# Kernel optimization log

Measured on AMD Instinct MI355X. Metric: run time of the kernel, lower is better.

Reference implementation:

```python
import math
import jax, jax.numpy as jnp
import numpy as np

N_LAYERS = 3

def _layer_masks(d):
    # Deterministic reproduction of generate_mask_matrix: mask_ratio = 0 for
    # layer < 2 else 1 - log(1/layer + 1); int(ratio*d) random dims zeroed.
    masks = []
    for layer in range(N_LAYERS):
        ratio = 0.0 if layer < 2 else 1.0 - math.log(1.0 / layer + 1.0)
        num_masked = int(ratio * d)
        perm = np.random.RandomState(layer).permutation(d)
        masks.append(jnp.asarray((perm >= num_masked).astype(np.float32)))
    return masks


def setup_inputs() -> dict:
    key = jax.random.key(0)
    ks = jax.random.split(key, 12)
    U, I, R, D, E, B = 50000, 50000, 5, 64, 1000000, 8192
    N = U + I
    return {
        "users": jax.random.randint(ks[0], (B,), 0, U, dtype=jnp.int32),
        "items": jax.random.randint(ks[1], (B,), 0, I, dtype=jnp.int32),
        "user_emb": jax.random.normal(ks[2], (U, D), dtype=jnp.float32) * 0.01,
        "item_emb": jax.random.normal(ks[3], (I, D), dtype=jnp.float32) * 0.01,
        "rating_emb": jax.random.normal(ks[4], (R, D), dtype=jnp.float32) * 0.01,
        "W1": jax.random.normal(ks[5], (R, 2 * D, D), dtype=jnp.float32) * (1.0 / math.sqrt(2 * D)),
        "b1": jnp.zeros((R, D), dtype=jnp.float32),
        "W2": jax.random.normal(ks[6], (R, D, D), dtype=jnp.float32) * (1.0 / math.sqrt(D)),
        "b2": jnp.zeros((R, D), dtype=jnp.float32),
        "rows": jax.random.randint(ks[7], (R, E), 0, N, dtype=jnp.int32),
        "cols": jax.random.randint(ks[8], (R, E), 0, N, dtype=jnp.int32),
        # normalized-adjacency-like positive values (~1/avg_degree)
        "vals": jax.random.uniform(ks[9], (R, E), dtype=jnp.float32) * 0.1,
    }


def reference(users, items, user_emb, item_emb, rating_emb, W1, b1, W2, b2, rows, cols, vals):
    U = user_emb.shape[0]
    N = U + item_emb.shape[0]
    R, D = rating_emb.shape
    masks = _layer_masks(D)

    base = jnp.concatenate([user_emb, item_emb], axis=0)  # [N, D]
    group_outs = []
    for r in range(R):  # fixed small set of rating groups
        # per-rating attention MLP on cat([emb, rating_emb_r])
        t = jnp.concatenate([base, jnp.broadcast_to(rating_emb[r], (N, D))], axis=1)  # [N, 2D]
        h = jax.nn.leaky_relu(t @ W1[r] + b1[r]) @ W2[r] + b2[r]  # [N, D]
        acc = h
        prev = h
        for layer in range(N_LAYERS):
            # sparse A @ prev via gather + segment_sum
            agg = jax.ops.segment_sum(vals[r][:, None] * prev[cols[r]], rows[r], num_segments=N)
            m = masks[layer]
            prev = agg * m + prev * (1.0 - m)  # diag-mask residual combine
            acc = acc + prev
        group_outs.append(acc)

    out = jnp.mean(jnp.stack(group_outs, axis=1), axis=1)  # agg == 'mean'
    users_emb = out[users]
    items_emb = out[U + items]
    return (users_emb * items_emb).sum(1)  # is_mlp = False
```

## Files before the change

kernel.cpp:

```cpp
#include <hip/hip_runtime.h>
#include <hip/hip_bf16.h>
#include <cstdint>
#include <cstddef>

#define KEYSHIFT 20
#define COLMASK 0xFFFFFu
#define EPB 8192
#define SUB 4096
#define BSHIFT 8
#define NRB 256
#define CCAP 3072

typedef short bf16x8 __attribute__((ext_vector_type(8)));
typedef float f32x4 __attribute__((ext_vector_type(4)));

__device__ __forceinline__ unsigned short f2bf(float f) {
    uint32_t u = __float_as_uint(f);
    u += ((u >> 16) & 1u) + 0x7fffu;
    return (unsigned short)(u >> 16);
}
__device__ __forceinline__ float bf2f(unsigned short h) {
    return __uint_as_float(((uint32_t)h) << 16);
}

static uint64_t compute_mask_bits() {
    uint32_t mt[624];
    mt[0] = 2u;
    for (int i = 1; i < 624; i++)
        mt[i] = 1812433253u * (mt[i - 1] ^ (mt[i - 1] >> 30)) + (uint32_t)i;
    int mti = 624;
    auto genrand = [&]() -> uint32_t {
        if (mti >= 624) {
            for (int k = 0; k < 624; k++) {
                uint32_t y = (mt[k] & 0x80000000u) | (mt[(k + 1) % 624] & 0x7fffffffu);
                mt[k] = mt[(k + 397) % 624] ^ (y >> 1) ^ ((y & 1u) ? 2567483615u : 0u);
            }
            mti = 0;
        }
        uint32_t y = mt[mti++];
        y ^= y >> 11;
        y ^= (y << 7) & 2636928640u;
        y ^= (y << 15) & 4022730752u;
        y ^= y >> 18;
        return y;
    };
    int arr[64];
    for (int i = 0; i < 64; i++) arr[i] = i;
    for (int i = 63; i >= 1; i--) {
        uint32_t mask = (uint32_t)i;
        mask |= mask >> 1; mask |= mask >> 2; mask |= mask >> 4;
        mask |= mask >> 8; mask |= mask >> 16;
        uint32_t v;
        do { v = genrand() & mask; } while (v > (uint32_t)i);
        int tmp = arr[i]; arr[i] = arr[v]; arr[v] = tmp;
    }
    uint64_t bits = 0;
    for (int d = 0; d < 64; d++)
        if (arr[d] >= 38) bits |= (1ull << d);
    return bits;
}

__global__ void flag_kernel(const int* __restrict__ users, const int* __restrict__ items,
                            unsigned char* __restrict__ flag, int B, int U) {
    int i = blockIdx.x * 256 + threadIdx.x;
    if (i < B) flag[users[i]] = 1;
    else if (i < 2 * B) flag[U + items[i - B]] = 1;
}

__global__ void flist_kernel(const unsigned char* __restrict__ flag,
                             int* __restrict__ flist, int* __restrict__ fcount, int n) {
    int i = blockIdx.x * 256 + threadIdx.x;
    if (i < n && flag[i]) {
        int p = atomicAdd(fcount, 1);
        flist[p] = i;
    }
}

__global__ void c1_kernel(const float* __restrict__ rating_emb, const float* __restrict__ W1,
                          const float* __restrict__ b1, float* __restrict__ c1_all) {
    int r = blockIdx.x;
    int t = threadIdx.x;
    const float* W1r = W1 + (size_t)r * (128 * 64);
    float acc = b1[r * 64 + t];
    for (int k = 0; k < 64; k++)
        acc += rating_emb[r * 64 + k] * W1r[(64 + k) * 64 + t];
    c1_all[r * 64 + t] = acc;
}

__global__ void packw_kernel(const float* __restrict__ W1, const float* __restrict__ W2,
                             short* __restrict__ wpack) {
    int r = blockIdx.x;
    int t = threadIdx.x;
    const float* W1r = W1 + (size_t)r * (128 * 64);
    const float* W2r = W2 + (size_t)r * (64 * 64);
    for (int e = t; e < 2 * 4 * 2 * 64 * 8; e += 256) {
        int i = e & 7;
        int lane = (e >> 3) & 63;
        int kc = (e >> 9) & 1;
        int ct = (e >> 10) & 3;
        int g = (e >> 12) & 1;
        int k = kc * 32 + ((lane >> 4) << 3) + i;
        int col = (ct << 4) + (lane & 15);
        float w = (g == 0) ? W1r[k * 64 + col] : W2r[k * 64 + col];
        unsigned short hi = f2bf(w);
        unsigned short lo = f2bf(w - bf2f(hi));
        size_t fb = ((((size_t)r * 2 + g) * 4 + ct) * 2 + kc) * 2;
        wpack[(fb + 0) * 512 + lane * 8 + i] = (short)hi;
        wpack[(fb + 1) * 512 + lane * 8 + i] = (short)lo;
    }
}

__global__ __launch_bounds__(1024) void bucket_count_kernel(
    const int* __restrict__ rows, int* __restrict__ gcnt,
    int* __restrict__ blockBase, int E, int K, int nb) {
    __shared__ int hist[2048];
    int r = blockIdx.y, blk = blockIdx.x, t = threadIdx.x;
    for (int i = t; i < K; i += 1024) hist[i] = 0;
    __syncthreads();
    size_t base = (size_t)r * E + (size_t)blk * EPB;
    int cnt = E - blk * EPB;
    if (cnt > EPB) cnt = EPB;
    for (int k = t; k < cnt; k += 1024)
        atomicAdd(&hist[rows[base + k] >> BSHIFT], 1);
    __syncthreads();
    for (int i = t; i < K; i += 1024) {
        int c = hist[i];
        int bb = (c > 0) ? atomicAdd(&gcnt[r * K + i], c) : 0;
        blockBase[((size_t)r * nb + blk) * K + i] = bb;
    }
}

__global__ void bucket_scan_kernel(const int* __restrict__ gcnt,
                                   int* __restrict__ bptr, int K) {
    __shared__ int sh[256];
    int r = blockIdx.x;
    int t = threadIdx.x;
    int base = t * 8;
    int v[8];
    int s = 0;
    #pragma unroll
    for (int j = 0; j < 8; j++) {
        int idx = base + j;
        v[j] = (idx < K) ? gcnt[r * K + idx] : 0;
        s += v[j];
    }
    sh[t] = s;
    __syncthreads();
    for (int off = 1; off < 256; off <<= 1) {
        int x = (t >= off) ? sh[t - off] : 0;
        __syncthreads();
        sh[t] += x;
        __syncthreads();
    }
    int run = sh[t] - s;
    #pragma unroll
    for (int j = 0; j < 8; j++) {
        int idx = base + j;
        if (idx <= K) bptr[r * (K + 1) + idx] = run;
        run += v[j];
    }
}

__global__ __launch_bounds__(1024) void bucket_scatter_kernel(
    const int* __restrict__ rows, const int* __restrict__ cols,
    const float* __restrict__ vals, const int* __restrict__ bptr,
    const int* __restrict__ blockBase, uint2* __restrict__ rec,
    int E, int K, long long eStride, long long pStride,
    long long bbStride, long long rStride) {
    __shared__ uint2 staged[SUB];
    __shared__ int gaddr[SUB];
    __shared__ int cursor[512];
    __shared__ int lhist[512];
    __shared__ int aux[512];
    int r = blockIdx.y;
    const int* rows_r = rows + (size_t)r * eStride;
    const int* cols_r = cols + (size_t)r * eStride;
    const float* vals_r = vals + (size_t)r * eStride;
    const int* bptr_r = bptr + (size_t)r * pStride;
    const int* bb_r = blockBase + (size_t)r * bbStride;
    uint2* rec_r = rec + (size_t)r * rStride;
    int blk = blockIdx.x, t = threadIdx.x;
    if (t < 512)
        cursor[t] = (t < K) ? (bptr_r[t] + bb_r[(size_t)blk * K + t]) : 0;
    size_t base = (size_t)blk * EPB;
    int cnt = E - blk * EPB;
    if (cnt > EPB) cnt = EPB;
    for (int c0 = 0; c0 < cnt; c0 += SUB) {
        int scnt = cnt - c0;
        if (scnt > SUB) scnt = SUB;
        if (t < 512) lhist[t] = 0;
        __syncthreads();
        int bkt_[4], lpos_[4];
        uint2 rv_[4];
        #pragma unroll
        for (int q = 0; q < 4; q++) {
            int kk = (q << 10) + t;
            bkt_[q] = -1;
            if (kk < scnt) {
                size_t g = base + c0 + kk;
                int row = rows_r[g];
                int b = row >> BSHIFT;
                bkt_[q] = b;
                rv_[q] = make_uint2(((uint32_t)(row & (NRB - 1)) << KEYSHIFT) |
                                        (uint32_t)cols_r[g],
                                    __float_as_uint(vals_r[g]));
                lpos_[q] = atomicAdd(&lhist[b], 1);
            }
        }
        __syncthreads();
        int v = (t < 512) ? lhist[t] : 0;
        if (t < 512) aux[t] = v;
        __syncthreads();
        for (int off = 1; off < 512; off <<= 1) {
            int x = 0;
            if (t >= off && t < 512) x = aux[t - off];
            __syncthreads();
            if (t < 512) aux[t] += x;
            __syncthreads();
        }
        if (t < 512) {
            int ex = aux[t] - v;
            int gb = cursor[t];
            cursor[t] = gb + v;
            lhist[t] = ex;
            aux[t] = gb - ex;
        }
        __syncthreads();
        #pragma unroll
        for (int q = 0; q < 4; q++) {
            if (bkt_[q] >= 0) {
                int sidx = lhist[bkt_[q]] + lpos_[q];
                staged[sidx] = rv_[q];
                gaddr[sidx] = aux[bkt_[q]] + sidx;
            }
        }
        __syncthreads();
        for (int i = t; i < scnt; i += 1024)
            rec_r[gaddr[i]] = staged[i];
        __syncthreads();
    }
}

__global__ __launch_bounds__(1024) void bucket_scatter_legacy(
    const int* __restrict__ rows, const int* __restrict__ cols,
    const float* __restrict__ vals, const int* __restrict__ bptr,
    const int* __restrict__ blockBase, uint2* __restrict__ rec,
    int E, int K, long long eStride, long long pStride,
    long long bbStride, long long rStride) {
    __shared__ int cursor[2048];
    int r = blockIdx.y;
    const int* rows_r = rows + (size_t)r * eStride;
    const int* cols_r = cols + (size_t)r * eStride;
    const float* vals_r = vals + (size_t)r * eStride;
    const int* bptr_r = bptr + (size_t)r * pStride;
    const int* bb_r = blockBase + (size_t)r * bbStride;
    uint2* rec_r = rec + (size_t)r * rStride;
    int blk = blockIdx.x, t = threadIdx.x;
    for (int i = t; i < K; i += 1024)
        cursor[i] = bptr_r[i] + bb_r[(size_t)blk * K + i];
    __syncthreads();
    size_t base = (size_t)blk * EPB;
    int cnt = E - blk * EPB;
    if (cnt > EPB) cnt = EPB;
    for (int k = t; k < cnt; k += 1024) {
        int row = rows_r[base + k];
        int b = row >> BSHIFT;
        int pos = atomicAdd(&cursor[b], 1);
        uint32_t key = ((uint32_t)(row & (NRB - 1)) << KEYSHIFT) | (uint32_t)cols_r[base + k];
        rec_r[pos] = make_uint2(key, __float_as_uint(vals_r[base + k]));
    }
}

__global__ __launch_bounds__(256) void bucket_sort_kernel(
    const uint2* __restrict__ rec, uint2* __restrict__ srec,
    const int* __restrict__ bptr, int* __restrict__ rp, int K, int N,
    long long rStride, long long pStride, long long rpStride) {
    __shared__ uint2 staged[CCAP];
    __shared__ int hist[NRB];
    __shared__ int excl[NRB];
    int r = blockIdx.y;
    const uint2* rec_r = rec + (size_t)r * rStride;
    uint2* srec_r = srec + (size_t)r * rStride;
    const int* bptr_r = bptr + (size_t)r * pStride;
    int* rp_r = rp + (size_t)r * rpStride;
    int b = blockIdx.x;
    int t = threadIdx.x;
    hist[t] = 0;
    __syncthreads();
    int start = bptr_r[b], end = bptr_r[b + 1];
    int m = end - start;
    for (int e = start + t; e < end; e += 256)
        atomicAdd(&hist[rec_r[e].x >> KEYSHIFT], 1);
    __syncthreads();
    int v = hist[t];
    excl[t] = v;
    __syncthreads();
    for (int off = 1; off < 256; off <<= 1) {
        int x = (t >= off) ? excl[t - off] : 0;
        __syncthreads();
        excl[t] += x;
        __syncthreads();
    }
    int ex = excl[t] - v;
    excl[t] = ex;
    hist[t] = 0;
    int row = b * NRB + t;
    if (row < N) rp_r[row] = start + ex;
    if (b == K - 1 && t == 0) rp_r[N] = bptr_r[K];
    __syncthreads();
    if (m <= CCAP) {
        for (int e = start + t; e < end; e += 256) {
            uint2 rr = rec_r[e];
            int rel = (int)(rr.x >> KEYSHIFT);
            int pos = excl[rel] + atomicAdd(&hist[rel], 1);
            staged[pos] = rr;
        }
        __syncthreads();
        for (int i = t; i < m; i += 256)
            srec_r[start + i] = staged[i];
    } else {
        for (int e = start + t; e < end; e += 256) {
            uint2 rr = rec_r[e];
            int rel = (int)(rr.x >> KEYSHIFT);
            int pos = start + excl[rel] + atomicAdd(&hist[rel], 1);
            srec_r[pos] = rr;
        }
    }
}

__global__ __launch_bounds__(256) void mlp_kernel(
    const float* __restrict__ user_emb, const float* __restrict__ item_emb,
    const short* __restrict__ wpack, const float* __restrict__ c1_all,
    const float* __restrict__ b2,
    unsigned short* __restrict__ prev, long long prevStride,
    float* __restrict__ out_acc, const unsigned char* __restrict__ flag,
    int r0, int nr, int n_rows, int U, int init) {
    __shared__ float sT[64 * 68];

    int t = threadIdx.x;
    int wv = t >> 6;
    int l = t & 63;
    int row0 = blockIdx.x * 64;
    int arow = row0 + (wv << 4) + (l & 15);
    int kb = (l >> 4) << 3;
    int trow = (wv << 4) + (l & 15);

    bf16x8 xh0, xh1, xl0, xl1;
    {
        float xv[16];
        #pragma unroll
        for (int i = 0; i < 16; i++) xv[i] = 0.f;
        if (arow < n_rows) {
            const float* src = (arow < U) ? (user_emb + (size_t)arow * 64)
                                          : (item_emb + (size_t)(arow - U) * 64);
            float4 p0 = *(const float4*)(src + kb);
            float4 p1 = *(const float4*)(src + kb + 4);
            float4 p2 = *(const float4*)(src + 32 + kb);
            float4 p3 = *(const float4*)(src + 32 + kb + 4);
            xv[0] = p0.x; xv[1] = p0.y; xv[2] = p0.z; xv[3] = p0.w;
            xv[4] = p1.x; xv[5] = p1.y; xv[6] = p1.z; xv[7] = p1.w;
            xv[8] = p2.x; xv[9] = p2.y; xv[10] = p2.z; xv[11] = p2.w;
            xv[12] = p3.x; xv[13] = p3.y; xv[14] = p3.z; xv[15] = p3.w;
        }
        #pragma unroll
        for (int i = 0; i < 8; i++) {
            unsigned short hi = f2bf(xv[i]);
            xh0[i] = (short)hi;
            xl0[i] = (short)f2bf(xv[i] - bf2f(hi));
        }
        #pragma unroll
        for (int i = 0; i < 8; i++) {
            unsigned short hi = f2bf(xv[8 + i]);
            xh1[i] = (short)hi;
            xl1[i] = (short)f2bf(xv[8 + i] - bf2f(hi));
        }
    }

    int dr0 = row0 + (wv << 4) + ((l >> 4) << 2);
    bool va0 = (dr0 + 0) < n_rows, va1 = (dr0 + 1) < n_rows;
    bool va2 = (dr0 + 2) < n_rows, va3 = (dr0 + 3) < n_rows;
    bool fl0 = va0 && flag[dr0 + 0], fl1 = va1 && flag[dr0 + 1];
    bool fl2 = va2 && flag[dr0 + 2], fl3 = va3 && flag[dr0 + 3];
    float oa[16];
    #pragma unroll
    for (int i = 0; i < 16; i++) oa[i] = 0.f;

    for (int rr = r0; rr < r0 + nr; ++rr) {
        const short* wp1 = wpack + ((size_t)rr * 2 + 0) * 16 * 512;
        const short* wp2 = wpack + ((size_t)rr * 2 + 1) * 16 * 512;

        #pragma unroll
        for (int ct = 0; ct < 4; ct++) {
            float c1v = c1_all[rr * 64 + (ct << 4) + (l & 15)];
            f32x4 acc = {c1v, c1v, c1v, c1v};
            #pragma unroll
            for (int kc = 0; kc < 2; kc++) {
                const short* fb = wp1 + ((ct * 2 + kc) * 2) * 512 + l * 8;
                bf16x8 bh = *(const bf16x8*)(fb);
                bf16x8 bl = *(const bf16x8*)(fb + 512);
                bf16x8 ah = (kc == 0) ? xh0 : xh1;
                bf16x8 al = (kc == 0) ? xl0 : xl1;
                acc = __builtin_amdgcn_mfma_f32_16x16x32_bf16(ah, bh, acc, 0, 0, 0);
                acc = __builtin_amdgcn_mfma_f32_16x16x32_bf16(al, bh, acc, 0, 0, 0);
                acc = __builtin_amdgcn_mfma_f32_16x16x32_bf16(ah, bl, acc, 0, 0, 0);
            }
            #pragma unroll
            for (int i = 0; i < 4; i++) {
                float v = acc[i];
                v = (v >= 0.f) ? v : 0.01f * v;
                sT[((wv << 4) + ((l >> 4) << 2) + i) * 68 + (ct << 4) + (l & 15)] = v;
            }
        }
        bf16x8 th0, th1, tl0, tl1;
        {
            float4 t0 = *(const float4*)(sT + trow * 68 + kb);
            float4 t1 = *(const float4*)(sT + trow * 68 + kb + 4);
            float4 t2 = *(const float4*)(sT + trow * 68 + 32 + kb);
            float4 t3 = *(const float4*)(sT + trow * 68 + 32 + kb + 4);
            float tv[16] = {t0.x, t0.y, t0.z, t0.w, t1.x, t1.y, t1.z, t1.w,
                            t2.x, t2.y, t2.z, t2.w, t3.x, t3.y, t3.z, t3.w};
            #pragma unroll
            for (int i = 0; i < 8; i++) {
                unsigned short hi = f2bf(tv[i]);
                th0[i] = (short)hi;
                tl0[i] = (short)f2bf(tv[i] - bf2f(hi));
            }
            #pragma unroll
            for (int i = 0; i < 8; i++) {
                unsigned short hi = f2bf(tv[8 + i]);
                th1[i] = (short)hi;
                tl1[i] = (short)f2bf(tv[8 + i] - bf2f(hi));
            }
        }
        #pragma unroll
        for (int ct = 0; ct < 4; ct++) {
            float b2v = b2[rr * 64 + (ct << 4) + (l & 15)];
            f32x4 acc = {b2v, b2v, b2v, b2v};
            #pragma unroll
            for (int kc = 0; kc < 2; kc++) {
                const short* fb = wp2 + ((ct * 2 + kc) * 2) * 512 + l * 8;
                bf16x8 bh = *(const bf16x8*)(fb);
                bf16x8 bl = *(const bf16x8*)(fb + 512);
                bf16x8 ah = (kc == 0) ? th0 : th1;
                bf16x8 al = (kc == 0) ? tl0 : tl1;
                acc = __builtin_amdgcn_mfma_f32_16x16x32_bf16(ah, bh, acc, 0, 0, 0);
                acc = __builtin_amdgcn_mfma_f32_16x16x32_bf16(al, bh, acc, 0, 0, 0);
                acc = __builtin_amdgcn_mfma_f32_16x16x32_bf16(ah, bl, acc, 0, 0, 0);
            }
            unsigned short* pp = prev + (size_t)rr * prevStride + (ct << 4) + (l & 15);
            #pragma unroll
            for (int i = 0; i < 4; i++) {
                bool va = (i == 0) ? va0 : (i == 1) ? va1 : (i == 2) ? va2 : va3;
                bool fl = (i == 0) ? fl0 : (i == 1) ? fl1 : (i == 2) ? fl2 : fl3;
                if (va) {
                    float hv = acc[i];
                    pp[(size_t)(dr0 + i) * 64] = f2bf(hv);
                    if (fl) oa[ct * 4 + i] += hv;
                }
            }
        }
    }

    #pragma unroll
    for (int ct = 0; ct < 4; ct++) {
        #pragma unroll
        for (int i = 0; i < 4; i++) {
            bool fl = (i == 0) ? fl0 : (i == 1) ? fl1 : (i == 2) ? fl2 : fl3;
            if (fl) {
                float* o = out_acc + (size_t)(dr0 + i) * 64 + (ct << 4) + (l & 15);
                if (init) *o = oa[ct * 4 + i];
                else *o += oa[ct * 4 + i];
            }
        }
    }
}

__global__ __launch_bounds__(256) void spmm_kernel(
    const unsigned short* __restrict__ prev, unsigned short* __restrict__ next,
    float* __restrict__ out_acc, const int* __restrict__ rp,
    const uint2* __restrict__ rec, const unsigned char* __restrict__ flag, int n) {
    int wave = (int)((blockIdx.x * (unsigned)blockDim.x + threadIdx.x) >> 6);
    int lane = threadIdx.x & 63;
    int rA = wave * 2;
    if (rA >= n) return;
    int rB = rA + 1;
    int sub = lane >> 4;
    int dl = lane & 15;
    int sA = rp[rA], eA = rp[rA + 1];
    int sB = 0, eB = 0;
    if (rB < n) { sB = rp[rB]; eB = rp[rB + 1]; }
    float axA = 0.f, ayA = 0.f, azA = 0.f, awA = 0.f;
    float axB = 0.f, ayB = 0.f, azB = 0.f, awB = 0.f;
    int ewA = sA + sub, ewB = sB + sub;
    while (ewA < eA || ewB < eB) {
        int a1 = ewA + 4, a2 = ewA + 8, a3 = ewA + 12;
        int b1 = ewB + 4, b2 = ewB + 8, b3 = ewB + 12;
        uint2 ra0 = rec[ewA < eA ? ewA : 0];
        uint2 ra1 = rec[a1 < eA ? a1 : 0];
        uint2 ra2 = rec[a2 < eA ? a2 : 0];
        uint2 ra3 = rec[a3 < eA ? a3 : 0];
        uint2 rb0 = rec[ewB < eB ? ewB : 0];
        uint2 rb1 = rec[b1 < eB ? b1 : 0];
        uint2 rb2 = rec[b2 < eB ? b2 : 0];
        uint2 rb3 = rec[b3 < eB ? b3 : 0];
        float vA0 = (ewA < eA) ? __uint_as_float(ra0.y) : 0.f;
        float vA1 = (a1 < eA) ? __uint_as_float(ra1.y) : 0.f;
        float vA2 = (a2 < eA) ? __uint_as_float(ra2.y) : 0.f;
        float vA3 = (a3 < eA) ? __uint_as_float(ra3.y) : 0.f;
        float vB0 = (ewB < eB) ? __uint_as_float(rb0.y) : 0.f;
        float vB1 = (b1 < eB) ? __uint_as_float(rb1.y) : 0.f;
        float vB2 = (b2 < eB) ? __uint_as_float(rb2.y) : 0.f;
        float vB3 = (b3 < eB) ? __uint_as_float(rb3.y) : 0.f;
        ushort4 qa0 = *(const ushort4*)(prev + (size_t)(ra0.x & COLMASK) * 64 + dl * 4);
        ushort4 qa1 = *(const ushort4*)(prev + (size_t)(ra1.x & COLMASK) * 64 + dl * 4);
        ushort4 qa2 = *(const ushort4*)(prev + (size_t)(ra2.x & COLMASK) * 64 + dl * 4);
        ushort4 qa3 = *(const ushort4*)(prev + (size_t)(ra3.x & COLMASK) * 64 + dl * 4);
        ushort4 qb0 = *(const ushort4*)(prev + (size_t)(rb0.x & COLMASK) * 64 + dl * 4);
        ushort4 qb1 = *(const ushort4*)(prev + (size_t)(rb1.x & COLMASK) * 64 + dl * 4);
        ushort4 qb2 = *(const ushort4*)(prev + (size_t)(rb2.x & COLMASK) * 64 + dl * 4);
        ushort4 qb3 = *(const ushort4*)(prev + (size_t)(rb3.x & COLMASK) * 64 + dl * 4);
        axA += vA0 * bf2f(qa0.x) + vA1 * bf2f(qa1.x) + vA2 * bf2f(qa2.x) + vA3 * bf2f(qa3.x);
        ayA += vA0 * bf2f(qa0.y) + vA1 * bf2f(qa1.y) + vA2 * bf2f(qa2.y) + vA3 * bf2f(qa3.y);
        azA += vA0 * bf2f(qa0.z) + vA1 * bf2f(qa1.z) + vA2 * bf2f(qa2.z) + vA3 * bf2f(qa3.z);
        awA += vA0 * bf2f(qa0.w) + vA1 * bf2f(qa1.w) + vA2 * bf2f(qa2.w) + vA3 * bf2f(qa3.w);
        axB += vB0 * bf2f(qb0.x) + vB1 * bf2f(qb1.x) + vB2 * bf2f(qb2.x) + vB3 * bf2f(qb3.x);
        ayB += vB0 * bf2f(qb0.y) + vB1 * bf2f(qb1.y) + vB2 * bf2f(qb2.y) + vB3 * bf2f(qb3.y);
        azB += vB0 * bf2f(qb0.z) + vB1 * bf2f(qb1.z) + vB2 * bf2f(qb2.z) + vB3 * bf2f(qb3.z);
        awB += vB0 * bf2f(qb0.w) + vB1 * bf2f(qb1.w) + vB2 * bf2f(qb2.w) + vB3 * bf2f(qb3.w);
        ewA += 16; ewB += 16;
    }
    axA += __shfl_xor(axA, 16); ayA += __shfl_xor(ayA, 16);
    azA += __shfl_xor(azA, 16); awA += __shfl_xor(awA, 16);
    axA += __shfl_xor(axA, 32); ayA += __shfl_xor(ayA, 32);
    azA += __shfl_xor(azA, 32); awA += __shfl_xor(awA, 32);
    axB += __shfl_xor(axB, 16); ayB += __shfl_xor(ayB, 16);
    azB += __shfl_xor(azB, 16); awB += __shfl_xor(awB, 16);
    axB += __shfl_xor(axB, 32); ayB += __shfl_xor(ayB, 32);
    azB += __shfl_xor(azB, 32); awB += __shfl_xor(awB, 32);
    if (sub == 0) {
        ushort4 nv;
        nv.x = f2bf(axA); nv.y = f2bf(ayA); nv.z = f2bf(azA); nv.w = f2bf(awA);
        *(ushort4*)(next + (size_t)rA * 64 + dl * 4) = nv;
    } else if (sub == 1 && flag[rA]) {
        float* o = out_acc + (size_t)rA * 64 + dl * 4;
        float4 ov = *(const float4*)o;
        ov.x += axA; ov.y += ayA; ov.z += azA; ov.w += awA;
        *(float4*)o = ov;
    } else if (sub == 2 && rB < n) {
        ushort4 nv;
        nv.x = f2bf(axB); nv.y = f2bf(ayB); nv.z = f2bf(azB); nv.w = f2bf(awB);
        *(ushort4*)(next + (size_t)rB * 64 + dl * 4) = nv;
    } else if (sub == 3 && rB < n && flag[rB]) {
        float* o = out_acc + (size_t)rB * 64 + dl * 4;
        float4 ov = *(const float4*)o;
        ov.x += axB; ov.y += ayB; ov.z += azB; ov.w += awB;
        *(float4*)o = ov;
    }
}

__global__ __launch_bounds__(256) void spmm_masked_kernel(
    const unsigned short* __restrict__ prev, float* __restrict__ out_acc,
    const int* __restrict__ rp, const uint2* __restrict__ rec,
    unsigned long long maskbits, const int* __restrict__ flist,
    const int* __restrict__ fcount) {
    int wave = (int)((blockIdx.x * (unsigned)blockDim.x + threadIdx.x) >> 6);
    int lane = threadIdx.x & 63;
    int fc = *fcount;
    int w2 = wave * 2;
    if (w2 >= fc) return;
    int rowA = flist[w2];
    int rowB = (w2 + 1 < fc) ? flist[w2 + 1] : -1;
    int sub = lane >> 4;
    int dl = lane & 15;
    int sA = rp[rowA], eA = rp[rowA + 1];
    int sB = 0, eB = 0;
    if (rowB >= 0) { sB = rp[rowB]; eB = rp[rowB + 1]; }
    float axA = 0.f, ayA = 0.f, azA = 0.f, awA = 0.f;
    float axB = 0.f, ayB = 0.f, azB = 0.f, awB = 0.f;
    int ewA = sA + sub, ewB = sB + sub;
    while (ewA < eA || ewB < eB) {
        int a1 = ewA + 4, a2 = ewA + 8, a3 = ewA + 12;
        int b1 = ewB + 4, b2 = ewB + 8, b3 = ewB + 12;
        uint2 ra0 = rec[ewA < eA ? ewA : 0];
        uint2 ra1 = rec[a1 < eA ? a1 : 0];
        uint2 ra2 = rec[a2 < eA ? a2 : 0];
        uint2 ra3 = rec[a3 < eA ? a3 : 0];
        uint2 rb0 = rec[ewB < eB ? ewB : 0];
        uint2 rb1 = rec[b1 < eB ? b1 : 0];
        uint2 rb2 = rec[b2 < eB ? b2 : 0];
        uint2 rb3 = rec[b3 < eB ? b3 : 0];
        float vA0 = (ewA < eA) ? __uint_as_float(ra0.y) : 0.f;
        float vA1 = (a1 < eA) ? __uint_as_float(ra1.y) : 0.f;
        float vA2 = (a2 < eA) ? __uint_as_float(ra2.y) : 0.f;
        float vA3 = (a3 < eA) ? __uint_as_float(ra3.y) : 0.f;
        float vB0 = (ewB < eB) ? __uint_as_float(rb0.y) : 0.f;
        float vB1 = (b1 < eB) ? __uint_as_float(rb1.y) : 0.f;
        float vB2 = (b2 < eB) ? __uint_as_float(rb2.y) : 0.f;
        float vB3 = (b3 < eB) ? __uint_as_float(rb3.y) : 0.f;
        ushort4 qa0 = *(const ushort4*)(prev + (size_t)(ra0.x & COLMASK) * 64 + dl * 4);
        ushort4 qa1 = *(const ushort4*)(prev + (size_t)(ra1.x & COLMASK) * 64 + dl * 4);
        ushort4 qa2 = *(const ushort4*)(prev + (size_t)(ra2.x & COLMASK) * 64 + dl * 4);
        ushort4 qa3 = *(const ushort4*)(prev + (size_t)(ra3.x & COLMASK) * 64 + dl * 4);
        ushort4 qb0 = *(const ushort4*)(prev + (size_t)(rb0.x & COLMASK) * 64 + dl * 4);
        ushort4 qb1 = *(const ushort4*)(prev + (size_t)(rb1.x & COLMASK) * 64 + dl * 4);
        ushort4 qb2 = *(const ushort4*)(prev + (size_t)(rb2.x & COLMASK) * 64 + dl * 4);
        ushort4 qb3 = *(const ushort4*)(prev + (size_t)(rb3.x & COLMASK) * 64 + dl * 4);
        axA += vA0 * bf2f(qa0.x) + vA1 * bf2f(qa1.x) + vA2 * bf2f(qa2.x) + vA3 * bf2f(qa3.x);
        ayA += vA0 * bf2f(qa0.y) + vA1 * bf2f(qa1.y) + vA2 * bf2f(qa2.y) + vA3 * bf2f(qa3.y);
        azA += vA0 * bf2f(qa0.z) + vA1 * bf2f(qa1.z) + vA2 * bf2f(qa2.z) + vA3 * bf2f(qa3.z);
        awA += vA0 * bf2f(qa0.w) + vA1 * bf2f(qa1.w) + vA2 * bf2f(qa2.w) + vA3 * bf2f(qa3.w);
        axB += vB0 * bf2f(qb0.x) + vB1 * bf2f(qb1.x) + vB2 * bf2f(qb2.x) + vB3 * bf2f(qb3.x);
        ayB += vB0 * bf2f(qb0.y) + vB1 * bf2f(qb1.y) + vB2 * bf2f(qb2.y) + vB3 * bf2f(qb3.y);
        azB += vB0 * bf2f(qb0.z) + vB1 * bf2f(qb1.z) + vB2 * bf2f(qb2.z) + vB3 * bf2f(qb3.z);
        awB += vB0 * bf2f(qb0.w) + vB1 * bf2f(qb1.w) + vB2 * bf2f(qb2.w) + vB3 * bf2f(qb3.w);
        ewA += 16; ewB += 16;
    }
    axA += __shfl_xor(axA, 16); ayA += __shfl_xor(ayA, 16);
    azA += __shfl_xor(azA, 16); awA += __shfl_xor(awA, 16);
    axA += __shfl_xor(axA, 32); ayA += __shfl_xor(ayA, 32);
    azA += __shfl_xor(azA, 32); awA += __shfl_xor(awA, 32);
    axB += __shfl_xor(axB, 16); ayB += __shfl_xor(ayB, 16);
    azB += __shfl_xor(azB, 16); awB += __shfl_xor(awB, 16);
    axB += __shfl_xor(axB, 32); ayB += __shfl_xor(ayB, 32);
    azB += __shfl_xor(azB, 32); awB += __shfl_xor(awB, 32);
    if (sub == 0) {
        ushort4 pq = *(const ushort4*)(prev + (size_t)rowA * 64 + dl * 4);
        float px = bf2f(pq.x), py = bf2f(pq.y), pz = bf2f(pq.z), pw = bf2f(pq.w);
        float rx = ((maskbits >> (dl * 4 + 0)) & 1ull) ? axA : px;
        float ry = ((maskbits >> (dl * 4 + 1)) & 1ull) ? ayA : py;
        float rz = ((maskbits >> (dl * 4 + 2)) & 1ull) ? azA : pz;
        float rw = ((maskbits >> (dl * 4 + 3)) & 1ull) ? awA : pw;
        float* o = out_acc + (size_t)rowA * 64 + dl * 4;
        float4 ov = *(const float4*)o;
        ov.x += rx; ov.y += ry; ov.z += rz; ov.w += rw;
        *(float4*)o = ov;
    } else if (sub == 2 && rowB >= 0) {
        ushort4 pq = *(const ushort4*)(prev + (size_t)rowB * 64 + dl * 4);
        float px = bf2f(pq.x), py = bf2f(pq.y), pz = bf2f(pq.z), pw = bf2f(pq.w);
        float rx = ((maskbits >> (dl * 4 + 0)) & 1ull) ? axB : px;
        float ry = ((maskbits >> (dl * 4 + 1)) & 1ull) ? ayB : py;
        float rz = ((maskbits >> (dl * 4 + 2)) & 1ull) ? azB : pz;
        float rw = ((maskbits >> (dl * 4 + 3)) & 1ull) ? awB : pw;
        float* o = out_acc + (size_t)rowB * 64 + dl * 4;
        float4 ov = *(const float4*)o;
        ov.x += rx; ov.y += ry; ov.z += rz; ov.w += rw;
        *(float4*)o = ov;
    }
}

__global__ __launch_bounds__(256) void dot_kernel(
    const float* __restrict__ out_acc, const int* __restrict__ users,
    const int* __restrict__ items, float* __restrict__ out,
    int Bn, int U, float scale) {
    int w = (int)((blockIdx.x * (unsigned)blockDim.x + threadIdx.x) >> 6);
    int lane = threadIdx.x & 63;
    if (w >= Bn) return;
    int u = users[w], it = items[w];
    float a = out_acc[(size_t)u * 64 + lane];
    float c = out_acc[((size_t)(U + it)) * 64 + lane];
    float p = a * c;
    #pragma unroll
    for (int off = 32; off > 0; off >>= 1) p += __shfl_down(p, off);
    if (lane == 0) out[w] = p * scale;
}

extern "C" void kernel_launch(void* const* d_in, const int* in_sizes, int n_in,
                              void* d_out, int out_size, void* d_ws, size_t ws_size,
                              hipStream_t stream) {
    const int* users = (const int*)d_in[0];
    const int* items = (const int*)d_in[1];
    const float* user_emb = (const float*)d_in[2];
    const float* item_emb = (const float*)d_in[3];
    const float* rating_emb = (const float*)d_in[4];
    const float* W1 = (const float*)d_in[5];
    const float* b1 = (const float*)d_in[6];
    const float* W2 = (const float*)d_in[7];
    const float* b2 = (const float*)d_in[8];
    const int* rows = (const int*)d_in[9];
    const int* cols = (const int*)d_in[10];
    const float* vals = (const float*)d_in[11];
    float* out = (float*)d_out;

    const int Dd = 64;
    int U = in_sizes[2] / Dd;
    int I = in_sizes[3] / Dd;
    int R = in_sizes[4] / Dd;
    int N = U + I;
    int E = in_sizes[9] / R;
    int Bn = in_sizes[0];
    int K = (N + NRB - 1) / NRB;
    int nb = (E + EPB - 1) / EPB;

    auto al = [](size_t b) { return (b + 255) & ~(size_t)255; };
    size_t sliceA = al((size_t)N * 64 * 2);
    size_t bufA_all = al((size_t)R * N * 64 * 2);
    size_t wpack_sz = al((size_t)R * 2 * 4 * 2 * 2 * 64 * 8 * 2);
    size_t common = al((size_t)N * 64 * 4) + sliceA
        + al((size_t)R * K * 4)
        + al((size_t)R * (K + 1) * 4) + al((size_t)R * nb * K * 4)
        + al((size_t)R * (N + 1) * 4) + al((size_t)R * 64 * 4) + wpack_sz
        + al((size_t)N) + al((size_t)2 * Bn * 4) + al(4);
    size_t rec_one = al((size_t)E * 8);
    size_t rec_all = al((size_t)E * 8 * R);
    int mlpb = 0, batched = 0;
    if (ws_size >= common + bufA_all + 2 * rec_all + 65536) {
        mlpb = 1; batched = 1;
    } else if (ws_size >= common + sliceA + 2 * rec_all + 65536) {
        batched = 1;
    }
    size_t bufAsz = mlpb ? bufA_all : sliceA;
    size_t recsz = batched ? rec_all : rec_one;

    char* p = (char*)d_ws;
    auto carve = [&](size_t bytes) -> char* {
        char* q = p;
        p += (bytes + 255) & ~(size_t)255;
        return q;
    };
    float* out_acc = (float*)carve((size_t)N * 64 * 4);
    unsigned short* bufA = (unsigned short*)carve(bufAsz);
    unsigned short* bufB = (unsigned short*)carve(sliceA);
    uint2* rec = (uint2*)carve(recsz);
    uint2* srec = (uint2*)carve(recsz);
    int* gcnt = (int*)carve((size_t)R * K * 4);
    int* bptr = (int*)carve((size_t)R * (K + 1) * 4);
    int* blockBase = (int*)carve((size_t)R * nb * K * 4);
    int* row_ptr = (int*)carve((size_t)R * (N + 1) * 4);
    float* c1_all = (float*)carve((size_t)R * 64 * 4);
    short* wpack = (short*)carve(wpack_sz);
    unsigned char* flag = (unsigned char*)carve((size_t)N);
    int* flist = (int*)carve((size_t)2 * Bn * 4);
    int* fcount = (int*)carve(4);

    uint64_t maskbits = compute_mask_bits();

    hipMemsetAsync(flag, 0, (size_t)N, stream);
    hipMemsetAsync(fcount, 0, 4, stream);
    hipMemsetAsync(gcnt, 0, (size_t)R * K * 4, stream);

    flag_kernel<<<(2 * Bn + 255) / 256, 256, 0, stream>>>(users, items, flag, Bn, U);
    flist_kernel<<<(N + 255) / 256, 256, 0, stream>>>(flag, flist, fcount, N);
    c1_kernel<<<R, 64, 0, stream>>>(rating_emb, W1, b1, c1_all);
    packw_kernel<<<R, 256, 0, stream>>>(W1, W2, wpack);

    dim3 cgrid(nb, R);
    bucket_count_kernel<<<cgrid, 1024, 0, stream>>>(rows, gcnt, blockBase, E, K, nb);
    bucket_scan_kernel<<<R, 256, 0, stream>>>(gcnt, bptr, K);

    if (batched) {
        dim3 sgrid(nb, R);
        if (K <= 512)
            bucket_scatter_kernel<<<sgrid, 1024, 0, stream>>>(
                rows, cols, vals, bptr, blockBase, rec, E, K,
                (long long)E, (long long)(K + 1), (long long)nb * K, (long long)E);
        else
            bucket_scatter_legacy<<<sgrid, 1024, 0, stream>>>(
                rows, cols, vals, bptr, blockBase, rec, E, K,
                (long long)E, (long long)(K + 1), (long long)nb * K, (long long)E);
        dim3 ogrid(K, R);
        bucket_sort_kernel<<<ogrid, 256, 0, stream>>>(
            rec, srec, bptr, row_ptr, K, N,
            (long long)E, (long long)(K + 1), (long long)(N + 1));
    }

    if (mlpb)
        mlp_kernel<<<(N + 63) / 64, 256, 0, stream>>>(
            user_emb, item_emb, wpack, c1_all, b2,
            bufA, (long long)N * 64, out_acc, flag, 0, R, N, U, 1);

    int spmm_waves = (N + 1) / 2;
    int spmm_blocks = (spmm_waves + 3) / 4;
    int masked_blocks = (Bn + 3) / 4;
    for (int r = 0; r < R; r++) {
        const int* bptr_r = bptr + (size_t)r * (K + 1);
        int* rp_r = row_ptr + (size_t)r * (N + 1);
        uint2* srec_r = batched ? (srec + (size_t)r * E) : srec;
        unsigned short* prev_r = mlpb ? (bufA + (size_t)r * N * 64) : bufA;

        if (!batched) {
            dim3 sgrid(nb, 1);
            if (K <= 512)
                bucket_scatter_kernel<<<sgrid, 1024, 0, stream>>>(
                    rows + (size_t)r * E, cols + (size_t)r * E, vals + (size_t)r * E,
                    bptr_r, blockBase + (size_t)r * nb * K, rec, E, K, 0, 0, 0, 0);
            else
                bucket_scatter_legacy<<<sgrid, 1024, 0, stream>>>(
                    rows + (size_t)r * E, cols + (size_t)r * E, vals + (size_t)r * E,
                    bptr_r, blockBase + (size_t)r * nb * K, rec, E, K, 0, 0, 0, 0);
            dim3 ogrid(K, 1);
            bucket_sort_kernel<<<ogrid, 256, 0, stream>>>(
                rec, srec, bptr_r, rp_r, K, N, 0, 0, 0);
        }

        if (!mlpb)
            mlp_kernel<<<(N + 63) / 64, 256, 0, stream>>>(
                user_emb, item_emb, wpack, c1_all, b2,
                bufA, 0, out_acc, flag, r, 1, N, U, (r == 0) ? 1 : 0);

        spmm_kernel<<<spmm_blocks, 256, 0, stream>>>(prev_r, bufB, out_acc, rp_r,
                                                     srec_r, flag, N);
        spmm_kernel<<<spmm_blocks, 256, 0, stream>>>(bufB, prev_r, out_acc, rp_r,
                                                     srec_r, flag, N);
        spmm_masked_kernel<<<masked_blocks, 256, 0, stream>>>(prev_r, out_acc, rp_r,
                                                              srec_r, maskbits,
                                                              flist, fcount);
    }

    float scale = 1.0f / (float)(R * R);
    dot_kernel<<<(Bn * 64 + 255) / 256, 256, 0, stream>>>(out_acc, users, items, out,
                                                          Bn, U, scale);
}
```

Measured before the change: 667.4 us.

## Batch SpMM across all rating groups in a 2D grid with deferred accumulation

When the workspace is large enough, the SpMM and masked SpMM launches for all five rating groups are merged into single launches, with blockIdx.y selecting the group. The out_acc read-modify-write that each group used to do is dropped from those kernels. Per-group results stay in full bufA/bufB buffers plus a compact masked-output buffer, and a new final_sum kernel adds them into out_acc for the flagged rows. This removes per-group launch overhead and serialization and fills the GPU with more concurrent work. In exchange it needs much more workspace and adds one extra reduction kernel.

```diff
diff --git a/kernel.cpp b/kernel.cpp
--- a/kernel.cpp
+++ b/kernel.cpp
@@ -478,7 +478,13 @@
 __global__ __launch_bounds__(256) void spmm_kernel(
     const unsigned short* __restrict__ prev, unsigned short* __restrict__ next,
     float* __restrict__ out_acc, const int* __restrict__ rp,
-    const uint2* __restrict__ rec, const unsigned char* __restrict__ flag, int n) {
+    const uint2* __restrict__ rec, const unsigned char* __restrict__ flag, int n,
+    long long pvS, long long nxS, long long rpS, long long rcS, int doOut) {
+    int rr = blockIdx.y;
+    prev += (size_t)rr * pvS;
+    next += (size_t)rr * nxS;
+    rp += (size_t)rr * rpS;
+    rec += (size_t)rr * rcS;
     int wave = (int)((blockIdx.x * (unsigned)blockDim.x + threadIdx.x) >> 6);
     int lane = threadIdx.x & 63;
     int rA = wave * 2;
@@ -541,7 +547,7 @@
         ushort4 nv;
         nv.x = f2bf(axA); nv.y = f2bf(ayA); nv.z = f2bf(azA); nv.w = f2bf(awA);
         *(ushort4*)(next + (size_t)rA * 64 + dl * 4) = nv;
-    } else if (sub == 1 && flag[rA]) {
+    } else if (sub == 1 && doOut && flag[rA]) {
         float* o = out_acc + (size_t)rA * 64 + dl * 4;
         float4 ov = *(const float4*)o;
         ov.x += axA; ov.y += ayA; ov.z += azA; ov.w += awA;
@@ -550,7 +556,7 @@
         ushort4 nv;
         nv.x = f2bf(axB); nv.y = f2bf(ayB); nv.z = f2bf(azB); nv.w = f2bf(awB);
         *(ushort4*)(next + (size_t)rB * 64 + dl * 4) = nv;
-    } else if (sub == 3 && rB < n && flag[rB]) {
+    } else if (sub == 3 && doOut && rB < n && flag[rB]) {
         float* o = out_acc + (size_t)rB * 64 + dl * 4;
         float4 ov = *(const float4*)o;
         ov.x += axB; ov.y += ayB; ov.z += azB; ov.w += awB;
@@ -562,7 +568,14 @@
     const unsigned short* __restrict__ prev, float* __restrict__ out_acc,
     const int* __restrict__ rp, const uint2* __restrict__ rec,
     unsigned long long maskbits, const int* __restrict__ flist,
-    const int* __restrict__ fcount) {
+    const int* __restrict__ fcount,
+    unsigned short* __restrict__ mout, long long moS,
+    long long pvS, long long rpS, long long rcS, int doOut) {
+    int rr = blockIdx.y;
+    prev += (size_t)rr * pvS;
+    rp += (size_t)rr * rpS;
+    rec += (size_t)rr * rcS;
+    unsigned short* mo = mout + (size_t)rr * moS;
     int wave = (int)((blockIdx.x * (unsigned)blockDim.x + threadIdx.x) >> 6);
     int lane = threadIdx.x & 63;
     int fc = *fcount;
@@ -630,10 +643,16 @@
         float ry = ((maskbits >> (dl * 4 + 1)) & 1ull) ? ayA : py;
         float rz = ((maskbits >> (dl * 4 + 2)) & 1ull) ? azA : pz;
         float rw = ((maskbits >> (dl * 4 + 3)) & 1ull) ? awA : pw;
-        float* o = out_acc + (size_t)rowA * 64 + dl * 4;
-        float4 ov = *(const float4*)o;
-        ov.x += rx; ov.y += ry; ov.z += rz; ov.w += rw;
-        *(float4*)o = ov;
+        if (doOut) {
+            float* o = out_acc + (size_t)rowA * 64 + dl * 4;
+            float4 ov = *(const float4*)o;
+            ov.x += rx; ov.y += ry; ov.z += rz; ov.w += rw;
+            *(float4*)o = ov;
+        } else {
+            ushort4 mv;
+            mv.x = f2bf(rx); mv.y = f2bf(ry); mv.z = f2bf(rz); mv.w = f2bf(rw);
+            *(ushort4*)(mo + (size_t)w2 * 64 + dl * 4) = mv;
+        }
     } else if (sub == 2 && rowB >= 0) {
         ushort4 pq = *(const ushort4*)(prev + (size_t)rowB * 64 + dl * 4);
         float px = bf2f(pq.x), py = bf2f(pq.y), pz = bf2f(pq.z), pw = bf2f(pq.w);
@@ -641,11 +660,35 @@
         float ry = ((maskbits >> (dl * 4 + 1)) & 1ull) ? ayB : py;
         float rz = ((maskbits >> (dl * 4 + 2)) & 1ull) ? azB : pz;
         float rw = ((maskbits >> (dl * 4 + 3)) & 1ull) ? awB : pw;
-        float* o = out_acc + (size_t)rowB * 64 + dl * 4;
-        float4 ov = *(const float4*)o;
-        ov.x += rx; ov.y += ry; ov.z += rz; ov.w += rw;
-        *(float4*)o = ov;
-    }
+        if (doOut) {
+            float* o = out_acc + (size_t)rowB * 64 + dl * 4;
+            float4 ov = *(const float4*)o;
+            ov.x += rx; ov.y += ry; ov.z += rz; ov.w += rw;
+            *(float4*)o = ov;
+        } else {
+            ushort4 mv;
+            mv.x = f2bf(rx); mv.y = f2bf(ry); mv.z = f2bf(rz); mv.w = f2bf(rw);
+            *(ushort4*)(mo + (size_t)(w2 + 1) * 64 + dl * 4) = mv;
+        }
+    }
+}
+
+__global__ __launch_bounds__(256) void final_sum_kernel(
+    float* __restrict__ out_acc, const unsigned short* __restrict__ bufA,
+    const unsigned short* __restrict__ bufB, const unsigned short* __restrict__ mout,
+    const int* __restrict__ flist, const int* __restrict__ fcount,
+    long long sliceS, long long moS, int R) {
+    int w = (int)((blockIdx.x * (unsigned)blockDim.x + threadIdx.x) >> 6);
+    int lane = threadIdx.x & 63;
+    if (w >= *fcount) return;
+    int row = flist[w];
+    float v = out_acc[(size_t)row * 64 + lane];
+    for (int r = 0; r < R; r++) {
+        v += bf2f(bufB[(size_t)r * sliceS + (size_t)row * 64 + lane]);
+        v += bf2f(bufA[(size_t)r * sliceS + (size_t)row * 64 + lane]);
+        v += bf2f(mout[(size_t)r * moS + (size_t)w * 64 + lane]);
+    }
+    out_acc[(size_t)row * 64 + lane] = v;
 }
 
 __global__ __launch_bounds__(256) void dot_kernel(
@@ -690,25 +733,29 @@
     int Bn = in_sizes[0];
     int K = (N + NRB - 1) / NRB;
     int nb = (E + EPB - 1) / EPB;
+    int maxF = 2 * Bn;
 
     auto al = [](size_t b) { return (b + 255) & ~(size_t)255; };
     size_t sliceA = al((size_t)N * 64 * 2);
     size_t bufA_all = al((size_t)R * N * 64 * 2);
+    size_t bufB_all = al((size_t)R * N * 64 * 2);
+    size_t mout_sz = al((size_t)R * maxF * 64 * 2);
     size_t wpack_sz = al((size_t)R * 2 * 4 * 2 * 2 * 64 * 8 * 2);
-    size_t common = al((size_t)N * 64 * 4) + sliceA
+    size_t common = al((size_t)N * 64 * 4)
         + al((size_t)R * K * 4)
         + al((size_t)R * (K + 1) * 4) + al((size_t)R * nb * K * 4)
         + al((size_t)R * (N + 1) * 4) + al((size_t)R * 64 * 4) + wpack_sz
         + al((size_t)N) + al((size_t)2 * Bn * 4) + al(4);
     size_t rec_one = al((size_t)E * 8);
     size_t rec_all = al((size_t)E * 8 * R);
-    int mlpb = 0, batched = 0;
-    if (ws_size >= common + bufA_all + 2 * rec_all + 65536) {
-        mlpb = 1; batched = 1;
-    } else if (ws_size >= common + sliceA + 2 * rec_all + 65536) {
-        batched = 1;
-    }
+    int tier = 0;
+    if (ws_size >= common + bufA_all + bufB_all + mout_sz + 2 * rec_all + 65536)
+        tier = 2;
+    else if (ws_size >= common + bufA_all + sliceA + 2 * rec_all + 65536)
+        tier = 1;
+    int mlpb = (tier >= 1), batched = (tier >= 1);
     size_t bufAsz = mlpb ? bufA_all : sliceA;
+    size_t bufBsz = (tier == 2) ? bufB_all : sliceA;
     size_t recsz = batched ? rec_all : rec_one;
 
     char* p = (char*)d_ws;
@@ -719,7 +766,8 @@
     };
     float* out_acc = (float*)carve((size_t)N * 64 * 4);
     unsigned short* bufA = (unsigned short*)carve(bufAsz);
-    unsigned short* bufB = (unsigned short*)carve(sliceA);
+    unsigned short* bufB = (unsigned short*)carve(bufBsz);
+    unsigned short* mout = (unsigned short*)carve((tier == 2) ? mout_sz : 0);
     uint2* rec = (uint2*)carve(recsz);
     uint2* srec = (uint2*)carve(recsz);
     int* gcnt = (int*)carve((size_t)R * K * 4);
@@ -771,39 +819,55 @@
     int spmm_waves = (N + 1) / 2;
     int spmm_blocks = (spmm_waves + 3) / 4;
     int masked_blocks = (Bn + 3) / 4;
-    for (int r = 0; r < R; r++) {
-        const int* bptr_r = bptr + (size_t)r * (K + 1);
-        int* rp_r = row_ptr + (size_t)r * (N + 1);
-        uint2* srec_r = batched ? (srec + (size_t)r * E) : srec;
-        unsigned short* prev_r = mlpb ? (bufA + (size_t)r * N * 64) : bufA;
-
-        if (!batched) {
-            dim3 sgrid(nb, 1);
-            if (K <= 512)
-                bucket_scatter_kernel<<<sgrid, 1024, 0, stream>>>(
-                    rows + (size_t)r * E, cols + (size_t)r * E, vals + (size_t)r * E,
-                    bptr_r, blockBase + (size_t)r * nb * K, rec, E, K, 0, 0, 0, 0);
-            else
-                bucket_scatter_legacy<<<sgrid, 1024, 0, stream>>>(
-                    rows + (size_t)r * E, cols + (size_t)r * E, vals + (size_t)r * E,
-                    bptr_r, blockBase + (size_t)r * nb * K, rec, E, K, 0, 0, 0, 0);
-            dim3 ogrid(K, 1);
-            bucket_sort_kernel<<<ogrid, 256, 0, stream>>>(
-                rec, srec, bptr_r, rp_r, K, N, 0, 0, 0);
-        }
-
-        if (!mlpb)
-            mlp_kernel<<<(N + 63) / 64, 256, 0, stream>>>(
-                user_emb, item_emb, wpack, c1_all, b2,
-                bufA, 0, out_acc, flag, r, 1, N, U, (r == 0) ? 1 : 0);
-
-        spmm_kernel<<<spmm_blocks, 256, 0, stream>>>(prev_r, bufB, out_acc, rp_r,
-                                                     srec_r, flag, N);
-        spmm_kernel<<<spmm_blocks, 256, 0, stream>>>(bufB, prev_r, out_acc, rp_r,
-                                                     srec_r, flag, N);
-        spmm_masked_kernel<<<masked_blocks, 256, 0, stream>>>(prev_r, out_acc, rp_r,
-                                                              srec_r, maskbits,
-                                                              flist, fcount);
+
+    if (tier == 2) {
+        long long slS = (long long)N * 64, rpS = (long long)(N + 1);
+        long long rcS = (long long)E, moS = (long long)maxF * 64;
+        dim3 g0(spmm_blocks, R), gm(masked_blocks, R);
+        spmm_kernel<<<g0, 256, 0, stream>>>(bufA, bufB, out_acc, row_ptr, srec,
+                                            flag, N, slS, slS, rpS, rcS, 0);
+        spmm_kernel<<<g0, 256, 0, stream>>>(bufB, bufA, out_acc, row_ptr, srec,
+                                            flag, N, slS, slS, rpS, rcS, 0);
+        spmm_masked_kernel<<<gm, 256, 0, stream>>>(bufA, out_acc, row_ptr, srec,
+                                                   maskbits, flist, fcount,
+                                                   mout, moS, slS, rpS, rcS, 0);
+        final_sum_kernel<<<(maxF * 64 + 255) / 256, 256, 0, stream>>>(
+            out_acc, bufA, bufB, mout, flist, fcount, slS, moS, R);
+    } else {
+        for (int r = 0; r < R; r++) {
+            const int* bptr_r = bptr + (size_t)r * (K + 1);
+            int* rp_r = row_ptr + (size_t)r * (N + 1);
+            uint2* srec_r = batched ? (srec + (size_t)r * E) : srec;
+            unsigned short* prev_r = mlpb ? (bufA + (size_t)r * N * 64) : bufA;
+
+            if (!batched) {
+                dim3 sgrid(nb, 1);
+                if (K <= 512)
+                    bucket_scatter_kernel<<<sgrid, 1024, 0, stream>>>(
+                        rows + (size_t)r * E, cols + (size_t)r * E, vals + (size_t)r * E,
+                        bptr_r, blockBase + (size_t)r * nb * K, rec, E, K, 0, 0, 0, 0);
+                else
+                    bucket_scatter_legacy<<<sgrid, 1024, 0, stream>>>(
+                        rows + (size_t)r * E, cols + (size_t)r * E, vals + (size_t)r * E,
+                        bptr_r, blockBase + (size_t)r * nb * K, rec, E, K, 0, 0, 0, 0);
+                dim3 ogrid(K, 1);
+                bucket_sort_kernel<<<ogrid, 256, 0, stream>>>(
+                    rec, srec, bptr_r, rp_r, K, N, 0, 0, 0);
+            }
+
+            if (!mlpb)
+                mlp_kernel<<<(N + 63) / 64, 256, 0, stream>>>(
+                    user_emb, item_emb, wpack, c1_all, b2,
+                    bufA, 0, out_acc, flag, r, 1, N, U, (r == 0) ? 1 : 0);
+
+            spmm_kernel<<<spmm_blocks, 256, 0, stream>>>(
+                prev_r, bufB, out_acc, rp_r, srec_r, flag, N, 0, 0, 0, 0, 1);
+            spmm_kernel<<<spmm_blocks, 256, 0, stream>>>(
+                bufB, prev_r, out_acc, rp_r, srec_r, flag, N, 0, 0, 0, 0, 1);
+            spmm_masked_kernel<<<masked_blocks, 256, 0, stream>>>(
+                prev_r, out_acc, rp_r, srec_r, maskbits, flist, fcount,
+                bufB , 0, 0, 0, 0, 1);
+        }
     }
 
     float scale = 1.0f / (float)(R * R);
```

Measured after the change: 605.1 us, median of 2. 9.3% less time.
